# Kernel tuning notes

Measured on AMD Instinct MI355X. Metric: run time of the kernel, lower is better.

The kernel has to match this reference:

```python
import jax, jax.numpy as jnp
import numpy as np

N, E, F_IN, HID, H1, H2, H3, OUT = 10000, 160000, 50, 350, 4, 4, 6, 121


def _gat(x, src, dst, n, W, a_s, a_d, b, heads, C, concat):
    # PyG GATConv (dropout=0, eval): h = xW^T reshaped to [N,H,C]
    h = (x @ W.T).reshape(n, heads, C)
    alpha_src = jnp.einsum('nhc,hc->nh', h, a_s)  # [N,H]
    alpha_dst = jnp.einsum('nhc,hc->nh', h, a_d)  # [N,H]
    e = jax.nn.leaky_relu(alpha_src[src] + alpha_dst[dst], 0.2)  # [E,H]
    # numerically-stable segment softmax over incoming edges of each dst node
    m = jax.ops.segment_max(e, dst, num_segments=n)
    ee = jnp.exp(e - m[dst])
    s = jax.ops.segment_sum(ee, dst, num_segments=n)
    alpha = ee / s[dst]  # self-loops guarantee s > 0
    out = jax.ops.segment_sum(h[src] * alpha[:, :, None], dst, num_segments=n)  # [N,H,C]
    out = out.reshape(n, heads * C) if concat else out.mean(axis=1)
    return out + b


def setup_inputs() -> dict:
    key = jax.random.key(0)
    ks = jax.random.split(key, 16)
    sc = 0.05
    inp = {
        'x': jax.random.normal(ks[0], (N, F_IN), dtype=jnp.float32),
        'edge_index': jax.random.randint(ks[1], (2, E), 0, N, dtype=jnp.int64) if jax.config.jax_enable_x64 else jax.random.randint(ks[1], (2, E), 0, N, dtype=jnp.int32),
        'W1': jax.random.normal(ks[2], (H1 * HID, F_IN), dtype=jnp.float32) * sc,
        'a1s': jax.random.normal(ks[3], (H1, HID), dtype=jnp.float32) * sc,
        'a1d': jax.random.normal(ks[4], (H1, HID), dtype=jnp.float32) * sc,
        'b1': jnp.zeros((H1 * HID,), dtype=jnp.float32),
        'W2': jax.random.normal(ks[5], (H2 * HID, H1 * HID), dtype=jnp.float32) * sc,
        'a2s': jax.random.normal(ks[6], (H2, HID), dtype=jnp.float32) * sc,
        'a2d': jax.random.normal(ks[7], (H2, HID), dtype=jnp.float32) * sc,
        'b2': jnp.zeros((H2 * HID,), dtype=jnp.float32),
        'Wskip': jax.random.normal(ks[8], (H2 * HID, H1 * HID), dtype=jnp.float32) * sc,
        'W3': jax.random.normal(ks[9], (H3 * OUT, H2 * HID), dtype=jnp.float32) * sc,
        'a3s': jax.random.normal(ks[10], (H3, OUT), dtype=jnp.float32) * sc,
        'a3d': jax.random.normal(ks[11], (H3, OUT), dtype=jnp.float32) * sc,
        'b3': jnp.zeros((OUT,), dtype=jnp.float32),
    }
    return inp


def reference(x, edge_index, W1, a1s, a1d, b1, W2, a2s, a2d, b2, Wskip, W3, a3s, a3d, b3):
    n = x.shape[0]
    loops = jnp.arange(n, dtype=edge_index.dtype)  # PyG add_self_loops=True
    src = jnp.concatenate([edge_index[0], loops])
    dst = jnp.concatenate([edge_index[1], loops])
    h = jax.nn.elu(_gat(x, src, dst, n, W1, a1s, a1d, b1, H1, HID, True))
    x_in = h
    h = jax.nn.elu(_gat(h, src, dst, n, W2, a2s, a2d, b2, H2, HID, True))
    h = h + x_in @ Wskip.T  # skip connection (bias=False)
    return _gat(h, src, dst, n, W3, a3s, a3d, b3, H3, OUT, False)
```

## Files before the change

kernel.cpp:

```cpp
#include <hip/hip_runtime.h>
#include <math.h>

#define NNODES 10000
#define NEDGES 160000
#define E2 (NEDGES + NNODES)
#define F_IN 50
#define HIDC 350
#define NH1 4
#define NH2 4
#define NH3 6
#define OUTC 121
#define MAXE 96
#define KP1 64
#define KP2 1408
#define LD3 736
#define ROWSLACK 128

typedef __attribute__((ext_vector_type(8))) short short8;
typedef __attribute__((ext_vector_type(8))) unsigned short ushort8v;
typedef __attribute__((ext_vector_type(4))) float floatx4;

static __device__ __forceinline__ unsigned short f2bf(float f) {
    unsigned u = __float_as_uint(f);
    unsigned r = (u + 0x7fffu + ((u >> 16) & 1u)) >> 16;
    return (unsigned short)r;
}
static __device__ __forceinline__ float bf2f(unsigned short s) {
    return __uint_as_float(((unsigned)s) << 16);
}

#define GLL16(gp, lp)                                                      \
    __builtin_amdgcn_global_load_lds(                                      \
        (const __attribute__((address_space(1))) void*)(gp),               \
        (__attribute__((address_space(3))) void*)(lp), 16, 0, 0)

__global__ void count_kernel(const int* __restrict__ ei, int* __restrict__ cnt) {
    int i = blockIdx.x * blockDim.x + threadIdx.x;
    if (i >= E2) return;
    int dst = (i < NEDGES) ? ei[NEDGES + i] : (i - NEDGES);
    atomicAdd(&cnt[dst], 1);
}

__global__ void scan_kernel(const int* __restrict__ cnt, int* __restrict__ indptr,
                            int* __restrict__ cursor) {
    __shared__ int part[1024];
    int tid = threadIdx.x;
    const int CH = (NNODES + 1023) / 1024;
    int base = tid * CH;
    int s = 0;
    for (int i = 0; i < CH; i++) {
        int idx = base + i;
        if (idx < NNODES) s += cnt[idx];
    }
    part[tid] = s;
    __syncthreads();
    for (int off = 1; off < 1024; off <<= 1) {
        int v = (tid >= off) ? part[tid - off] : 0;
        __syncthreads();
        part[tid] += v;
        __syncthreads();
    }
    int run = (tid == 0) ? 0 : part[tid - 1];
    for (int i = 0; i < CH; i++) {
        int idx = base + i;
        if (idx < NNODES) {
            indptr[idx] = run;
            cursor[idx] = run;
            run += cnt[idx];
        }
    }
    if (tid == 0) indptr[NNODES] = part[1023];
}

__global__ void scatter_kernel(const int* __restrict__ ei, int* __restrict__ cursor,
                               int* __restrict__ esrc) {
    int i = blockIdx.x * blockDim.x + threadIdx.x;
    if (i >= E2) return;
    int src, dst;
    if (i < NEDGES) {
        src = ei[i];
        dst = ei[NEDGES + i];
    } else {
        src = dst = i - NEDGES;
    }
    int pos = atomicAdd(&cursor[dst], 1);
    esrc[pos] = src;
}

__global__ void splitW1_kernel(const float* __restrict__ W1,
                               unsigned short* __restrict__ w1Hi,
                               unsigned short* __restrict__ w1Lo) {
    int k = threadIdx.x;
    int r = blockIdx.x;
    float v = (k < F_IN) ? W1[(size_t)r * F_IN + k] : 0.f;
    unsigned short h = f2bf(v);
    w1Hi[(size_t)r * KP1 + k] = h;
    w1Lo[(size_t)r * KP1 + k] = f2bf(v - bf2f(h));
}

__global__ void splitB_kernel(const float* __restrict__ W2, const float* __restrict__ Wsk,
                              const float* __restrict__ W3,
                              unsigned short* __restrict__ w2Hi,
                              unsigned short* __restrict__ w3Hi) {
    int k = blockIdx.x * blockDim.x + threadIdx.x;
    if (k >= KP2) return;
    int r = blockIdx.y;
    const int K = 1400;
    const float* src;
    unsigned short* hi;
    int row;
    if (r < 1400) { src = W2; row = r; hi = w2Hi; }
    else if (r < 2800) { src = Wsk; row = r - 1400; hi = w2Hi + (size_t)1400 * KP2; }
    else { src = W3; row = r - 2800; hi = w3Hi; }
    float v = (k < K) ? src[(size_t)row * K + k] : 0.f;
    hi[(size_t)row * KP2 + k] = f2bf(v);
}

__global__ void atil_kernel(const float* __restrict__ W, const float* __restrict__ av_s,
                            const float* __restrict__ av_d, float* __restrict__ outS,
                            float* __restrict__ outD, int C, int K, int cchunk) {
    int k = blockIdx.x * 64 + (threadIdx.x & 63);
    if (k >= K) return;
    int h = blockIdx.y;
    int c0 = blockIdx.z * cchunk;
    int c1 = c0 + cchunk;
    if (c1 > C) c1 = C;
    float ss = 0.f, dd = 0.f;
    for (int c = c0; c < c1; c++) {
        float wv = W[((size_t)h * C + c) * K + k];
        ss = fmaf(wv, av_s[h * C + c], ss);
        dd = fmaf(wv, av_d[h * C + c], dd);
    }
    atomicAdd(&outS[(size_t)h * K + k], ss);
    atomicAdd(&outD[(size_t)h * K + k], dd);
}

__global__ void splitAT2_kernel(const float* __restrict__ atall,
                                unsigned short* __restrict__ atHi,
                                unsigned short* __restrict__ atLo) {
    int k = blockIdx.x * 64 + threadIdx.x;
    int r = blockIdx.y;
    float v = 0.f;
    if (k < 1400) {
        if (r < 4) v = atall[400 + r * 1400 + k];
        else if (r < 8) v = atall[6000 + (r - 4) * 1400 + k];
    }
    unsigned short h = f2bf(v);
    atHi[(size_t)r * KP2 + k] = h;
    atLo[(size_t)r * KP2 + k] = f2bf(v - bf2f(h));
}

__global__ __launch_bounds__(256) void alpha1x_kernel(const float* __restrict__ x,
                                                      const float* __restrict__ at1s,
                                                      const float* __restrict__ at1d,
                                                      float* __restrict__ as1,
                                                      float* __restrict__ ad1) {
    int wave = threadIdx.x >> 6, lane = threadIdx.x & 63;
    int n = blockIdx.x * 4 + wave;
    if (n >= NNODES) return;
    int kk = lane < F_IN ? lane : F_IN - 1;
    float v = (lane < F_IN) ? x[(size_t)n * F_IN + lane] : 0.f;
    float p[8];
#pragma unroll
    for (int h = 0; h < 4; h++) {
        p[h] = v * at1s[h * F_IN + kk];
        p[4 + h] = v * at1d[h * F_IN + kk];
    }
#pragma unroll
    for (int s = 0; s < 8; s++)
#pragma unroll
        for (int o = 32; o > 0; o >>= 1) p[s] += __shfl_xor(p[s], o, 64);
    if (lane == 0) {
#pragma unroll
        for (int h = 0; h < 4; h++) {
            as1[n * 4 + h] = p[h];
            ad1[n * 4 + h] = p[4 + h];
        }
    }
}

__global__ void zeropad_kernel(unsigned short* __restrict__ hi) {
    int i = blockIdx.x * 256 + threadIdx.x;
    if (i >= NNODES * 8) return;
    int n = i >> 3, c = 1400 + (i & 7);
    hi[(size_t)n * KP2 + c] = 0;
}

__global__ __launch_bounds__(256) void agg_x(
    const float* __restrict__ x, const float* __restrict__ as_n,
    const float* __restrict__ ad_n, const int* __restrict__ indptr,
    const int* __restrict__ esrc, unsigned short* __restrict__ xaggHi,
    unsigned short* __restrict__ xaggLo) {
    int n = blockIdx.x, tid = threadIdx.x;
    int s = indptr[n], e = indptr[n + 1];
    int deg = e - s;
    if (deg > MAXE) deg = MAXE;
    __shared__ int srcs[MAXE];
    __shared__ float wgt[MAXE * 4];

    if (tid < 64) {
        int lane = tid;
        float adv[4], mx[4], sm[4];
#pragma unroll
        for (int h = 0; h < 4; h++) {
            adv[h] = ad_n[n * 4 + h];
            mx[h] = -1e30f;
            sm[h] = 0.f;
        }
        for (int j = lane; j < deg; j += 64) {
            int sr = esrc[s + j];
            srcs[j] = sr;
#pragma unroll
            for (int h = 0; h < 4; h++) {
                float ev = as_n[sr * 4 + h] + adv[h];
                ev = ev > 0.f ? ev : 0.2f * ev;
                wgt[j * 4 + h] = ev;
                mx[h] = fmaxf(mx[h], ev);
            }
        }
#pragma unroll
        for (int h = 0; h < 4; h++)
#pragma unroll
            for (int o = 32; o > 0; o >>= 1) mx[h] = fmaxf(mx[h], __shfl_xor(mx[h], o, 64));
        for (int j = lane; j < deg; j += 64) {
#pragma unroll
            for (int h = 0; h < 4; h++) {
                float p = __expf(wgt[j * 4 + h] - mx[h]);
                wgt[j * 4 + h] = p;
                sm[h] += p;
            }
        }
#pragma unroll
        for (int h = 0; h < 4; h++) {
#pragma unroll
            for (int o = 32; o > 0; o >>= 1) sm[h] += __shfl_xor(sm[h], o, 64);
            sm[h] = 1.f / sm[h];
        }
        for (int j = lane; j < deg; j += 64) {
#pragma unroll
            for (int h = 0; h < 4; h++) wgt[j * 4 + h] *= sm[h];
        }
    }
    __syncthreads();

    int h = tid >> 6, k = tid & 63;
    float a = 0.f;
    if (k < F_IN) {
        float a2 = 0.f;
        int j = 0;
        for (; j + 1 < deg; j += 2) {
            a = fmaf(wgt[j * 4 + h], x[(size_t)srcs[j] * F_IN + k], a);
            a2 = fmaf(wgt[(j + 1) * 4 + h], x[(size_t)srcs[j + 1] * F_IN + k], a2);
        }
        if (j < deg) a = fmaf(wgt[j * 4 + h], x[(size_t)srcs[j] * F_IN + k], a);
        a += a2;
    }
    unsigned short hi = f2bf(a);
    xaggHi[(size_t)n * 256 + tid] = hi;
    xaggLo[(size_t)n * 256 + tid] = f2bf(a - bf2f(hi));
}

__global__ __launch_bounds__(256, 2) void gemm_h1(
    const unsigned short* __restrict__ xaggHi, const unsigned short* __restrict__ xaggLo,
    const unsigned short* __restrict__ w1Hi, const unsigned short* __restrict__ w1Lo,
    const float* __restrict__ bias, unsigned short* __restrict__ actHi) {
    __shared__ __align__(16) unsigned short sA[2][128 * 32];
    __shared__ __align__(16) unsigned short sB[2][256 * 32];
    int tid = threadIdx.x;
    int wave = tid >> 6, lane = tid & 63;
    int wm = (wave >> 1) * 64, wn = (wave & 1) * 128;
    int fr = lane & 15, kq = lane >> 4;
    int row0 = blockIdx.y * 128, col0 = blockIdx.x * 256;
    int hd = blockIdx.z;

    floatx4 acc[4][8];
#pragma unroll
    for (int i = 0; i < 4; i++)
#pragma unroll
        for (int j = 0; j < 8; j++)
#pragma unroll
            for (int q = 0; q < 4; q++) acc[i][j][q] = 0.f;

    int gpos = lane & 3;
    int rl = lane >> 2;
    int gsw = kq ^ ((fr >> 1) & 3);

    for (int k0 = 0; k0 < 64; k0 += 32) {
#pragma unroll
        for (int c = 0; c < 2; ++c) {
            int r = wave * 32 + c * 16 + rl;
            int g = gpos ^ ((r >> 1) & 3);
            size_t gofs = (size_t)(row0 + r) * 256 + hd * 64 + k0 + g * 8;
            size_t lofs = (size_t)r * 32 + (size_t)gpos * 8;
            GLL16(xaggHi + gofs, &sA[0][lofs]);
            GLL16(xaggLo + gofs, &sA[1][lofs]);
        }
#pragma unroll
        for (int c = 0; c < 4; ++c) {
            int r = wave * 64 + c * 16 + rl;
            int g = gpos ^ ((r >> 1) & 3);
            size_t gofs = (size_t)(hd * 350 + col0 + r) * KP1 + k0 + g * 8;
            size_t lofs = (size_t)r * 32 + (size_t)gpos * 8;
            GLL16(w1Hi + gofs, &sB[0][lofs]);
            GLL16(w1Lo + gofs, &sB[1][lofs]);
        }
        __syncthreads();

        short8 ah[4], al[4], bh[8], bl[8];
#pragma unroll
        for (int j = 0; j < 8; j++) {
            int rb = wn + j * 16 + fr;
            bh[j] = *(const short8*)&sB[0][rb * 32 + gsw * 8];
            bl[j] = *(const short8*)&sB[1][rb * 32 + gsw * 8];
        }
#pragma unroll
        for (int i = 0; i < 4; i++) {
            int ra = wm + i * 16 + fr;
            ah[i] = *(const short8*)&sA[0][ra * 32 + gsw * 8];
            al[i] = *(const short8*)&sA[1][ra * 32 + gsw * 8];
        }
#pragma unroll
        for (int i = 0; i < 4; i++)
#pragma unroll
            for (int j = 0; j < 8; j++) {
                acc[i][j] = __builtin_amdgcn_mfma_f32_16x16x32_bf16(ah[i], bh[j],
                                                                   acc[i][j], 0, 0, 0);
                acc[i][j] = __builtin_amdgcn_mfma_f32_16x16x32_bf16(al[i], bh[j],
                                                                   acc[i][j], 0, 0, 0);
                acc[i][j] = __builtin_amdgcn_mfma_f32_16x16x32_bf16(ah[i], bl[j],
                                                                   acc[i][j], 0, 0, 0);
            }
        __syncthreads();
    }

#pragma unroll
    for (int i = 0; i < 4; i++) {
#pragma unroll
        for (int rg = 0; rg < 4; rg++) {
            int rr = row0 + wm + i * 16 + kq * 4 + rg;
            if (rr >= NNODES) continue;
#pragma unroll
            for (int j = 0; j < 8; j++) {
                int cc = col0 + wn + j * 16 + fr;
                if (cc < 350) {
                    int gc = hd * 350 + cc;
                    float v = acc[i][j][rg] + bias[gc];
                    v = v > 0.f ? v : expm1f(v);
                    actHi[(size_t)rr * KP2 + gc] = f2bf(v);
                }
            }
        }
    }
}

__global__ __launch_bounds__(256) void alpha_mfma(
    const unsigned short* __restrict__ act, const unsigned short* __restrict__ tHi,
    const unsigned short* __restrict__ tLo, int H, float* __restrict__ asx,
    float* __restrict__ adx) {
    int wave = threadIdx.x >> 6, lane = threadIdx.x & 63;
    int row0 = (blockIdx.x * 4 + wave) * 16;
    if (row0 >= NNODES) return;
    int fr = lane & 15, kq = lane >> 4;
    floatx4 acc = {0.f, 0.f, 0.f, 0.f};
    const unsigned short* arow = act + (size_t)(row0 + fr) * KP2 + kq * 8;
    const unsigned short* brh = tHi + (size_t)fr * KP2 + kq * 8;
    const unsigned short* brl = tLo + (size_t)fr * KP2 + kq * 8;
#pragma unroll 4
    for (int k0 = 0; k0 < KP2; k0 += 32) {
        short8 a = *(const short8*)(arow + k0);
        short8 vh = *(const short8*)(brh + k0);
        short8 vl = *(const short8*)(brl + k0);
        acc = __builtin_amdgcn_mfma_f32_16x16x32_bf16(a, vh, acc, 0, 0, 0);
        acc = __builtin_amdgcn_mfma_f32_16x16x32_bf16(a, vl, acc, 0, 0, 0);
    }
#pragma unroll
    for (int rg = 0; rg < 4; rg++) {
        int rr = row0 + kq * 4 + rg;
        if (fr < H) asx[rr * H + fr] = acc[rg];
        else if (fr < 2 * H) adx[rr * H + (fr - H)] = acc[rg];
    }
}

__global__ __launch_bounds__(256, 2) void gemm_b16(
    const unsigned short* __restrict__ A, const unsigned short* __restrict__ B,
    unsigned short* __restrict__ Cb, int NN, int M, int Kp, int ldc) {
    __shared__ __align__(16) unsigned short sA[128 * 32];
    __shared__ __align__(16) unsigned short sB[256 * 32];
    int tid = threadIdx.x;
    int wave = tid >> 6, lane = tid & 63;
    int wm = (wave >> 1) * 64, wn = (wave & 1) * 128;
    int fr = lane & 15, kq = lane >> 4;
    int row0 = blockIdx.y * 128, col0 = blockIdx.x * 256;

    floatx4 acc[4][8];
#pragma unroll
    for (int i = 0; i < 4; i++)
#pragma unroll
        for (int j = 0; j < 8; j++)
#pragma unroll
            for (int q = 0; q < 4; q++) acc[i][j][q] = 0.f;

    int gpos = lane & 3;
    int rl = lane >> 2;
    int gsw = kq ^ ((fr >> 1) & 3);

    for (int k0 = 0; k0 < Kp; k0 += 32) {
#pragma unroll
        for (int c = 0; c < 2; ++c) {
            int r = wave * 32 + c * 16 + rl;
            int g = gpos ^ ((r >> 1) & 3);
            GLL16(A + (size_t)(row0 + r) * Kp + k0 + g * 8,
                  &sA[(size_t)r * 32 + (size_t)gpos * 8]);
        }
#pragma unroll
        for (int c = 0; c < 4; ++c) {
            int r = wave * 64 + c * 16 + rl;
            int g = gpos ^ ((r >> 1) & 3);
            GLL16(B + (size_t)(col0 + r) * Kp + k0 + g * 8,
                  &sB[(size_t)r * 32 + (size_t)gpos * 8]);
        }
        __syncthreads();

        short8 ah[4], bh[8];
#pragma unroll
        for (int j = 0; j < 8; j++) {
            int rb = wn + j * 16 + fr;
            bh[j] = *(const short8*)&sB[rb * 32 + gsw * 8];
        }
#pragma unroll
        for (int i = 0; i < 4; i++) {
            int ra = wm + i * 16 + fr;
            ah[i] = *(const short8*)&sA[ra * 32 + gsw * 8];
        }
#pragma unroll
        for (int i = 0; i < 4; i++)
#pragma unroll
            for (int j = 0; j < 8; j++)
                acc[i][j] = __builtin_amdgcn_mfma_f32_16x16x32_bf16(ah[i], bh[j],
                                                                   acc[i][j], 0, 0, 0);
        __syncthreads();
    }

#pragma unroll
    for (int i = 0; i < 4; i++) {
#pragma unroll
        for (int rg = 0; rg < 4; rg++) {
            int rr = row0 + wm + i * 16 + kq * 4 + rg;
            if (rr >= NN) continue;
#pragma unroll
            for (int j = 0; j < 8; j++) {
                int cc = col0 + wn + j * 16 + fr;
                if (cc < M) Cb[(size_t)rr * ldc + cc] = f2bf(acc[i][j][rg]);
            }
        }
    }
}

#define AGG_T 192
template <int H, int C, int MODE, int DOELU, int SKIP, int HN>
__global__ __launch_bounds__(AGG_T) void agg2(
    const unsigned short* __restrict__ hpreb, int ldh,
    const float* __restrict__ as_n, const float* __restrict__ ad_n,
    const int* __restrict__ indptr, const int* __restrict__ esrc,
    const float* __restrict__ bias, unsigned short* __restrict__ outHi, int Kp,
    float* __restrict__ outF, const float* __restrict__ atns,
    const float* __restrict__ atnd, float* __restrict__ asx,
    float* __restrict__ adx) {
    constexpr int HC = H * C;
    int n = blockIdx.x;
    int tid = threadIdx.x;
    int s = indptr[n], e = indptr[n + 1];
    int deg = e - s;
    if (deg > MAXE) deg = MAXE;

    __shared__ int srcs[MAXE];
    __shared__ float wgt[MAXE * H];
    __shared__ float aggsh[MODE ? HC : 1];
    __shared__ float sAl[16];
    if (tid < 16) sAl[tid] = 0.f;

    if (tid < 64) {
        int lane = tid;
        float adv[H], mx[H], sm[H];
#pragma unroll
        for (int h = 0; h < H; h++) {
            adv[h] = ad_n[n * H + h];
            mx[h] = -1e30f;
            sm[h] = 0.f;
        }
        for (int j = lane; j < deg; j += 64) {
            int sr = esrc[s + j];
            srcs[j] = sr;
#pragma unroll
            for (int h = 0; h < H; h++) {
                float ev = as_n[sr * H + h] + adv[h];
                ev = ev > 0.f ? ev : 0.2f * ev;
                wgt[j * H + h] = ev;
                mx[h] = fmaxf(mx[h], ev);
            }
        }
#pragma unroll
        for (int h = 0; h < H; h++)
#pragma unroll
            for (int o = 32; o > 0; o >>= 1) mx[h] = fmaxf(mx[h], __shfl_xor(mx[h], o, 64));
        for (int j = lane; j < deg; j += 64) {
#pragma unroll
            for (int h = 0; h < H; h++) {
                float p = __expf(wgt[j * H + h] - mx[h]);
                wgt[j * H + h] = p;
                sm[h] += p;
            }
        }
#pragma unroll
        for (int h = 0; h < H; h++) {
#pragma unroll
            for (int o = 32; o > 0; o >>= 1) sm[h] += __shfl_xor(sm[h], o, 64);
            sm[h] = 1.f / sm[h];
        }
        for (int j = lane; j < deg; j += 64) {
#pragma unroll
            for (int h = 0; h < H; h++) wgt[j * H + h] *= sm[h];
        }
    }
    __syncthreads();

    if (MODE == 0) {
        constexpr int NV8 = HC / 8;
        constexpr int NP = (HN > 0) ? 2 * HN : 1;
        float p[NP];
#pragma unroll
        for (int q = 0; q < NP; q++) p[q] = 0.f;

        for (int c8 = tid; c8 < NV8; c8 += AGG_T) {
            int cb = c8 * 8;
            int h0 = cb / C;
            int sp = (h0 + 1) * C - cb;
            if (sp > 8) sp = 8;
            int h1 = (h0 + 1 < H) ? h0 + 1 : h0;
            float av[8];
#pragma unroll
            for (int q = 0; q < 8; q++) av[q] = 0.f;
            int j = 0;
            for (; j + 3 < deg; j += 4) {
                const ushort8v v0 = *(const ushort8v*)(hpreb + (size_t)srcs[j] * ldh + cb);
                const ushort8v v1 = *(const ushort8v*)(hpreb + (size_t)srcs[j + 1] * ldh + cb);
                const ushort8v v2 = *(const ushort8v*)(hpreb + (size_t)srcs[j + 2] * ldh + cb);
                const ushort8v v3 = *(const ushort8v*)(hpreb + (size_t)srcs[j + 3] * ldh + cb);
                float wa0 = wgt[j * H + h0], wa1 = wgt[j * H + h1];
                float wb0 = wgt[(j + 1) * H + h0], wb1 = wgt[(j + 1) * H + h1];
                float wc0 = wgt[(j + 2) * H + h0], wc1 = wgt[(j + 2) * H + h1];
                float wd0 = wgt[(j + 3) * H + h0], wd1 = wgt[(j + 3) * H + h1];
#pragma unroll
                for (int q = 0; q < 8; q++) av[q] = fmaf(q < sp ? wa0 : wa1, bf2f(v0[q]), av[q]);
#pragma unroll
                for (int q = 0; q < 8; q++) av[q] = fmaf(q < sp ? wb0 : wb1, bf2f(v1[q]), av[q]);
#pragma unroll
                for (int q = 0; q < 8; q++) av[q] = fmaf(q < sp ? wc0 : wc1, bf2f(v2[q]), av[q]);
#pragma unroll
                for (int q = 0; q < 8; q++) av[q] = fmaf(q < sp ? wd0 : wd1, bf2f(v3[q]), av[q]);
            }
            for (; j < deg; j++) {
                const ushort8v v0 = *(const ushort8v*)(hpreb + (size_t)srcs[j] * ldh + cb);
                float wa0 = wgt[j * H + h0], wa1 = wgt[j * H + h1];
#pragma unroll
                for (int q = 0; q < 8; q++) av[q] = fmaf(q < sp ? wa0 : wa1, bf2f(v0[q]), av[q]);
            }
#pragma unroll
            for (int q = 0; q < 8; q++) av[q] += bias[cb + q];
            if (DOELU) {
#pragma unroll
                for (int q = 0; q < 8; q++) av[q] = av[q] > 0.f ? av[q] : expm1f(av[q]);
            }
            if (SKIP) {
                const ushort8v sk = *(const ushort8v*)(hpreb + (size_t)n * ldh + 1400 + cb);
#pragma unroll
                for (int q = 0; q < 8; q++) av[q] += bf2f(sk[q]);
            }
            if (HN > 0) {
#pragma unroll
                for (int h = 0; h < HN; h++) {
                    float ss = 0.f, dd = 0.f;
#pragma unroll
                    for (int q = 0; q < 8; q++) {
                        ss = fmaf(av[q], atns[(size_t)h * HC + cb + q], ss);
                        dd = fmaf(av[q], atnd[(size_t)h * HC + cb + q], dd);
                    }
                    p[h] += ss;
                    p[HN + h] += dd;
                }
            }
            ushort8v hi8;
#pragma unroll
            for (int q = 0; q < 8; q++) hi8[q] = f2bf(av[q]);
            *(ushort8v*)(outHi + (size_t)n * Kp + cb) = hi8;
        }
        for (int c = HC + tid; c < Kp; c += AGG_T) outHi[(size_t)n * Kp + c] = 0;
        if (HN > 0) {
#pragma unroll
            for (int q = 0; q < NP; q++)
#pragma unroll
                for (int o = 32; o > 0; o >>= 1) p[q] += __shfl_xor(p[q], o, 64);
            if ((tid & 63) == 0) {
#pragma unroll
                for (int q = 0; q < NP; q++) atomicAdd(&sAl[q], p[q]);
            }
            __syncthreads();
            if (tid < HN) asx[n * HN + tid] = sAl[tid];
            else if (tid < 2 * HN) adx[n * HN + (tid - HN)] = sAl[tid];
        }
    } else {
        constexpr int NV8 = (HC + 7) / 8;
        for (int c8 = tid; c8 < NV8; c8 += AGG_T) {
            int cb = c8 * 8;
            int h0 = cb / C;
            if (h0 >= H) h0 = H - 1;
            int sp = (h0 + 1) * C - cb;
            if (sp > 8) sp = 8;
            int h1 = (h0 + 1 < H) ? h0 + 1 : h0;
            float av[8];
#pragma unroll
            for (int q = 0; q < 8; q++) av[q] = 0.f;
            int j = 0;
            for (; j + 3 < deg; j += 4) {
                const ushort8v v0 = *(const ushort8v*)(hpreb + (size_t)srcs[j] * ldh + cb);
                const ushort8v v1 = *(const ushort8v*)(hpreb + (size_t)srcs[j + 1] * ldh + cb);
                const ushort8v v2 = *(const ushort8v*)(hpreb + (size_t)srcs[j + 2] * ldh + cb);
                const ushort8v v3 = *(const ushort8v*)(hpreb + (size_t)srcs[j + 3] * ldh + cb);
                float wa0 = wgt[j * H + h0], wa1 = wgt[j * H + h1];
                float wb0 = wgt[(j + 1) * H + h0], wb1 = wgt[(j + 1) * H + h1];
                float wc0 = wgt[(j + 2) * H + h0], wc1 = wgt[(j + 2) * H + h1];
                float wd0 = wgt[(j + 3) * H + h0], wd1 = wgt[(j + 3) * H + h1];
#pragma unroll
                for (int q = 0; q < 8; q++) av[q] = fmaf(q < sp ? wa0 : wa1, bf2f(v0[q]), av[q]);
#pragma unroll
                for (int q = 0; q < 8; q++) av[q] = fmaf(q < sp ? wb0 : wb1, bf2f(v1[q]), av[q]);
#pragma unroll
                for (int q = 0; q < 8; q++) av[q] = fmaf(q < sp ? wc0 : wc1, bf2f(v2[q]), av[q]);
#pragma unroll
                for (int q = 0; q < 8; q++) av[q] = fmaf(q < sp ? wd0 : wd1, bf2f(v3[q]), av[q]);
            }
            for (; j < deg; j++) {
                const ushort8v v0 = *(const ushort8v*)(hpreb + (size_t)srcs[j] * ldh + cb);
                float wa0 = wgt[j * H + h0], wa1 = wgt[j * H + h1];
#pragma unroll
                for (int q = 0; q < 8; q++) av[q] = fmaf(q < sp ? wa0 : wa1, bf2f(v0[q]), av[q]);
            }
#pragma unroll
            for (int q = 0; q < 8; q++)
                if (cb + q < HC) aggsh[cb + q] = av[q];
        }
        __syncthreads();
        for (int c = tid; c < C; c += AGG_T) {
            float sres = 0.f;
#pragma unroll
            for (int h = 0; h < H; h++) sres += aggsh[h * C + c];
            outF[(size_t)n * C + c] = sres * (1.f / (float)H) + bias[c];
        }
    }
}

extern "C" void kernel_launch(void* const* d_in, const int* in_sizes, int n_in,
                              void* d_out, int out_size, void* d_ws, size_t ws_size,
                              hipStream_t stream) {
    const float* x = (const float*)d_in[0];
    const int* ei = (const int*)d_in[1];
    const float* W1 = (const float*)d_in[2];
    const float* a1s = (const float*)d_in[3];
    const float* a1d = (const float*)d_in[4];
    const float* b1 = (const float*)d_in[5];
    const float* W2 = (const float*)d_in[6];
    const float* a2s = (const float*)d_in[7];
    const float* a2d = (const float*)d_in[8];
    const float* b2 = (const float*)d_in[9];
    const float* Wsk = (const float*)d_in[10];
    const float* W3 = (const float*)d_in[11];
    const float* a3s = (const float*)d_in[12];
    const float* a3d = (const float*)d_in[13];
    const float* b3 = (const float*)d_in[14];
    float* out = (float*)d_out;

    char* w = (char*)d_ws;
    size_t off = 0;
    auto alloc = [&](size_t bytes) -> char* {
        char* p = w + off;
        off += (bytes + 255) & ~(size_t)255;
        return p;
    };
    unsigned short* hpreb = (unsigned short*)alloc((size_t)(NNODES + ROWSLACK) * 2800 * 2);
    unsigned short* actHi = (unsigned short*)alloc((size_t)(NNODES + ROWSLACK) * KP2 * 2);
    unsigned short* xaggHi = (unsigned short*)alloc((size_t)(NNODES + ROWSLACK) * 256 * 2);
    unsigned short* xaggLo = (unsigned short*)alloc((size_t)(NNODES + ROWSLACK) * 256 * 2);
    unsigned short* w1Hi = (unsigned short*)alloc((size_t)(1400 + 512) * KP1 * 2);
    unsigned short* w1Lo = (unsigned short*)alloc((size_t)(1400 + 512) * KP1 * 2);
    unsigned short* w2Hi = (unsigned short*)alloc((size_t)(2800 + ROWSLACK) * KP2 * 2);
    unsigned short* w3Hi = (unsigned short*)alloc((size_t)(726 + ROWSLACK) * KP2 * 2);
    unsigned short* at2Hi = (unsigned short*)alloc((size_t)16 * KP2 * 2);
    unsigned short* at2Lo = (unsigned short*)alloc((size_t)16 * KP2 * 2);
    float* atall = (float*)alloc((size_t)28400 * 4);
    int* cnt = (int*)alloc((size_t)(NNODES + 16) * 4);
    float* at1s = atall;
    float* at1d = atall + 200;
    float* at2s = atall + 400;
    float* at2d = atall + 6000;
    float* at3s = atall + 11600;
    float* at3d = atall + 20000;
    float* asP = (float*)alloc((size_t)NNODES * 6 * 4);
    float* adP = (float*)alloc((size_t)NNODES * 6 * 4);
    float* asQ = (float*)alloc((size_t)NNODES * 6 * 4);
    float* adQ = (float*)alloc((size_t)NNODES * 6 * 4);
    int* indptr = (int*)alloc((size_t)(NNODES + 16) * 4);
    int* cursor = (int*)alloc((size_t)(NNODES + 16) * 4);
    int* esrc = (int*)alloc((size_t)E2 * 4);

    size_t zbytes = (size_t)((char*)cnt - (char*)atall) + (NNODES + 16) * 4;
    hipMemsetAsync(atall, 0, zbytes, stream);

    splitW1_kernel<<<1400, 64, 0, stream>>>(W1, w1Hi, w1Lo);
    splitB_kernel<<<dim3(6, 2800 + 726), 256, 0, stream>>>(W2, Wsk, W3, w2Hi, w3Hi);
    atil_kernel<<<dim3(1, 4, 5), 64, 0, stream>>>(W1, a1s, a1d, at1s, at1d, HIDC, F_IN, 70);
    atil_kernel<<<dim3(22, 4, 5), 64, 0, stream>>>(W2, a2s, a2d, at2s, at2d, HIDC, 1400, 70);
    atil_kernel<<<dim3(22, 6, 4), 64, 0, stream>>>(W3, a3s, a3d, at3s, at3d, OUTC, 1400, 31);
    splitAT2_kernel<<<dim3(22, 16), 64, 0, stream>>>(atall, at2Hi, at2Lo);
    alpha1x_kernel<<<(NNODES + 3) / 4, 256, 0, stream>>>(x, at1s, at1d, asP, adP);

    count_kernel<<<(E2 + 255) / 256, 256, 0, stream>>>(ei, cnt);
    scan_kernel<<<1, 1024, 0, stream>>>(cnt, indptr, cursor);
    scatter_kernel<<<(E2 + 255) / 256, 256, 0, stream>>>(ei, cursor, esrc);

    zeropad_kernel<<<(NNODES * 8 + 255) / 256, 256, 0, stream>>>(actHi);

    dim3 blk(256);
    int gy = (NNODES + 127) / 128;

    agg_x<<<NNODES, 256, 0, stream>>>(x, asP, adP, indptr, esrc, xaggHi, xaggLo);
    gemm_h1<<<dim3(2, gy, 4), blk, 0, stream>>>(xaggHi, xaggLo, w1Hi, w1Lo, b1, actHi);
    alpha_mfma<<<(NNODES / 16 + 3) / 4, 256, 0, stream>>>(actHi, at2Hi, at2Lo, 4, asQ, adQ);

    {
        int M = 2800;
        dim3 grid((M + 255) / 256, gy);
        gemm_b16<<<grid, blk, 0, stream>>>(actHi, w2Hi, hpreb, NNODES, M, KP2, 2800);
        agg2<NH2, HIDC, 0, 1, 1, 6><<<NNODES, AGG_T, 0, stream>>>(
            hpreb, 2800, asQ, adQ, indptr, esrc, b2, actHi, KP2, nullptr,
            at3s, at3d, asP, adP);
    }
    {
        int M = NH3 * OUTC;
        dim3 grid((M + 255) / 256, gy);
        gemm_b16<<<grid, blk, 0, stream>>>(actHi, w3Hi, hpreb, NNODES, M, KP2, LD3);
        agg2<NH3, OUTC, 1, 0, 0, 0><<<NNODES, AGG_T, 0, stream>>>(
            hpreb, LD3, asP, adP, indptr, esrc, b3, nullptr, 0, out,
            nullptr, nullptr, nullptr, nullptr);
    }
}
```

Measured before the change: 635.1 us.

## Precompute edge softmax weights in separate kernel and remap GEMM blocks across XCDs

The per-node edge softmax moves out of the aggregation kernels into a separate alpha_edge kernel that writes normalized weights to a global buffer. The aggregation kernels then just load those weights, so all threads start gathering at once instead of waiting for a single wave to finish the softmax. gemm_b16 also remaps block IDs so that consecutive tiles land on the same XCD, which is meant to improve L2 reuse. The cost is extra kernel launches and an extra global write and read of the per-edge weights.

```diff
diff --git a/kernel.cpp b/kernel.cpp
--- a/kernel.cpp
+++ b/kernel.cpp
@@ -381,6 +381,61 @@
     }
 }
 
+template <int H>
+__global__ __launch_bounds__(64) void alpha_edge(
+    const float* __restrict__ as_n, const float* __restrict__ ad_n,
+    const int* __restrict__ indptr, const int* __restrict__ esrc,
+    float* __restrict__ walpha) {
+    int n = blockIdx.x;
+    int lane = threadIdx.x;
+    int s = indptr[n], e = indptr[n + 1];
+    int deg = e - s;
+    if (deg > MAXE) deg = MAXE;
+    __shared__ float wgt[MAXE * H];
+    float adv[H], mx[H], sm[H];
+#pragma unroll
+    for (int h = 0; h < H; h++) {
+        adv[h] = ad_n[n * H + h];
+        mx[h] = -1e30f;
+        sm[h] = 0.f;
+    }
+    for (int j = lane; j < deg; j += 64) {
+        int sr = esrc[s + j];
+#pragma unroll
+        for (int h = 0; h < H; h++) {
+            float ev = as_n[sr * H + h] + adv[h];
+            ev = ev > 0.f ? ev : 0.2f * ev;
+            wgt[j * H + h] = ev;
+            mx[h] = fmaxf(mx[h], ev);
+        }
+    }
+#pragma unroll
+    for (int h = 0; h < H; h++)
+#pragma unroll
+        for (int o = 32; o > 0; o >>= 1) mx[h] = fmaxf(mx[h], __shfl_xor(mx[h], o, 64));
+    for (int j = lane; j < deg; j += 64) {
+#pragma unroll
+        for (int h = 0; h < H; h++) {
+            float p = __expf(wgt[j * H + h] - mx[h]);
+            wgt[j * H + h] = p;
+            sm[h] += p;
+        }
+    }
+#pragma unroll
+    for (int h = 0; h < H; h++) {
+#pragma unroll
+        for (int o = 32; o > 0; o >>= 1) sm[h] += __shfl_xor(sm[h], o, 64);
+        sm[h] = 1.f / sm[h];
+    }
+    for (int j = lane; j < deg; j += 64) {
+#pragma unroll
+        for (int h = 0; h < H; h++) wgt[j * H + h] *= sm[h];
+    }
+    __syncthreads();
+    for (int i = lane; i < deg * H; i += 64)
+        walpha[(size_t)s * H + i] = wgt[i];
+}
+
 __global__ __launch_bounds__(256, 2) void gemm_b16(
     const unsigned short* __restrict__ A, const unsigned short* __restrict__ B,
     unsigned short* __restrict__ Cb, int NN, int M, int Kp, int ldc) {
@@ -390,7 +445,14 @@
     int wave = tid >> 6, lane = tid & 63;
     int wm = (wave >> 1) * 64, wn = (wave & 1) * 128;
     int fr = lane & 15, kq = lane >> 4;
-    int row0 = blockIdx.y * 128, col0 = blockIdx.x * 256;
+
+    int gx = (int)gridDim.x;
+    int nwg = gx * (int)gridDim.y;
+    int bid = (int)blockIdx.y * gx + (int)blockIdx.x;
+    int qq = nwg >> 3, rr8 = nwg & 7;
+    int xcd = bid & 7, idx = bid >> 3;
+    int nb = (xcd < rr8) ? xcd * (qq + 1) + idx : rr8 * (qq + 1) + (xcd - rr8) * qq + idx;
+    int row0 = (nb / gx) * 128, col0 = (nb % gx) * 256;
 
     floatx4 acc[4][8];
 #pragma unroll
@@ -445,27 +507,122 @@
     for (int i = 0; i < 4; i++) {
 #pragma unroll
         for (int rg = 0; rg < 4; rg++) {
-            int rr = row0 + wm + i * 16 + kq * 4 + rg;
-            if (rr >= NN) continue;
+            int rrow = row0 + wm + i * 16 + kq * 4 + rg;
+            if (rrow >= NN) continue;
 #pragma unroll
             for (int j = 0; j < 8; j++) {
                 int cc = col0 + wn + j * 16 + fr;
-                if (cc < M) Cb[(size_t)rr * ldc + cc] = f2bf(acc[i][j][rg]);
+                if (cc < M) Cb[(size_t)rrow * ldc + cc] = f2bf(acc[i][j][rg]);
             }
         }
     }
 }
 
 #define AGG_T 192
-template <int H, int C, int MODE, int DOELU, int SKIP, int HN>
 __global__ __launch_bounds__(AGG_T) void agg2(
     const unsigned short* __restrict__ hpreb, int ldh,
-    const float* __restrict__ as_n, const float* __restrict__ ad_n,
     const int* __restrict__ indptr, const int* __restrict__ esrc,
-    const float* __restrict__ bias, unsigned short* __restrict__ outHi, int Kp,
-    float* __restrict__ outF, const float* __restrict__ atns,
-    const float* __restrict__ atnd, float* __restrict__ asx,
-    float* __restrict__ adx) {
+    const float* __restrict__ walpha, const float* __restrict__ bias,
+    unsigned short* __restrict__ outHi, int Kp,
+    const float* __restrict__ atns, const float* __restrict__ atnd,
+    float* __restrict__ asx, float* __restrict__ adx) {
+    constexpr int H = 4, C = 350, HC = 1400, HN = 6;
+    int n = blockIdx.x;
+    int tid = threadIdx.x;
+    int s = indptr[n], e = indptr[n + 1];
+    int deg = e - s;
+    if (deg > MAXE) deg = MAXE;
+
+    __shared__ int srcs[MAXE];
+    __shared__ float wgt[MAXE * H];
+    __shared__ float sAl[16];
+    if (tid < 16) sAl[tid] = 0.f;
+    for (int i = tid; i < deg; i += AGG_T) srcs[i] = esrc[s + i];
+    for (int i = tid; i < deg * H; i += AGG_T) wgt[i] = walpha[(size_t)s * H + i];
+    __syncthreads();
+
+    constexpr int NV8 = HC / 8;
+    float p[2 * HN];
+#pragma unroll
+    for (int q = 0; q < 2 * HN; q++) p[q] = 0.f;
+
+    for (int c8 = tid; c8 < NV8; c8 += AGG_T) {
+        int cb = c8 * 8;
+        int h0 = cb / C;
+        int sp = (h0 + 1) * C - cb;
+        if (sp > 8) sp = 8;
+        int h1 = (h0 + 1 < H) ? h0 + 1 : h0;
+        float av[8];
+#pragma unroll
+        for (int q = 0; q < 8; q++) av[q] = 0.f;
+        int j = 0;
+        for (; j + 3 < deg; j += 4) {
+            const ushort8v v0 = *(const ushort8v*)(hpreb + (size_t)srcs[j] * ldh + cb);
+            const ushort8v v1 = *(const ushort8v*)(hpreb + (size_t)srcs[j + 1] * ldh + cb);
+            const ushort8v v2 = *(const ushort8v*)(hpreb + (size_t)srcs[j + 2] * ldh + cb);
+            const ushort8v v3 = *(const ushort8v*)(hpreb + (size_t)srcs[j + 3] * ldh + cb);
+            float wa0 = wgt[j * H + h0], wa1 = wgt[j * H + h1];
+            float wb0 = wgt[(j + 1) * H + h0], wb1 = wgt[(j + 1) * H + h1];
+            float wc0 = wgt[(j + 2) * H + h0], wc1 = wgt[(j + 2) * H + h1];
+            float wd0 = wgt[(j + 3) * H + h0], wd1 = wgt[(j + 3) * H + h1];
+#pragma unroll
+            for (int q = 0; q < 8; q++) av[q] = fmaf(q < sp ? wa0 : wa1, bf2f(v0[q]), av[q]);
+#pragma unroll
+            for (int q = 0; q < 8; q++) av[q] = fmaf(q < sp ? wb0 : wb1, bf2f(v1[q]), av[q]);
+#pragma unroll
+            for (int q = 0; q < 8; q++) av[q] = fmaf(q < sp ? wc0 : wc1, bf2f(v2[q]), av[q]);
+#pragma unroll
+            for (int q = 0; q < 8; q++) av[q] = fmaf(q < sp ? wd0 : wd1, bf2f(v3[q]), av[q]);
+        }
+        for (; j < deg; j++) {
+            const ushort8v v0 = *(const ushort8v*)(hpreb + (size_t)srcs[j] * ldh + cb);
+            float wa0 = wgt[j * H + h0], wa1 = wgt[j * H + h1];
+#pragma unroll
+            for (int q = 0; q < 8; q++) av[q] = fmaf(q < sp ? wa0 : wa1, bf2f(v0[q]), av[q]);
+        }
+#pragma unroll
+        for (int q = 0; q < 8; q++) av[q] += bias[cb + q];
+#pragma unroll
+        for (int q = 0; q < 8; q++) av[q] = av[q] > 0.f ? av[q] : expm1f(av[q]);
+        const ushort8v sk = *(const ushort8v*)(hpreb + (size_t)n * ldh + 1400 + cb);
+#pragma unroll
+        for (int q = 0; q < 8; q++) av[q] += bf2f(sk[q]);
+#pragma unroll
+        for (int h = 0; h < HN; h++) {
+            float ss = 0.f, dd = 0.f;
+#pragma unroll
+            for (int q = 0; q < 8; q++) {
+                ss = fmaf(av[q], atns[(size_t)h * HC + cb + q], ss);
+                dd = fmaf(av[q], atnd[(size_t)h * HC + cb + q], dd);
+            }
+            p[h] += ss;
+            p[HN + h] += dd;
+        }
+        ushort8v hi8;
+#pragma unroll
+        for (int q = 0; q < 8; q++) hi8[q] = f2bf(av[q]);
+        *(ushort8v*)(outHi + (size_t)n * Kp + cb) = hi8;
+    }
+    for (int c = HC + tid; c < Kp; c += AGG_T) outHi[(size_t)n * Kp + c] = 0;
+#pragma unroll
+    for (int q = 0; q < 2 * HN; q++)
+#pragma unroll
+        for (int o = 32; o > 0; o >>= 1) p[q] += __shfl_xor(p[q], o, 64);
+    if ((tid & 63) == 0) {
+#pragma unroll
+        for (int q = 0; q < 2 * HN; q++) atomicAdd(&sAl[q], p[q]);
+    }
+    __syncthreads();
+    if (tid < HN) asx[n * HN + tid] = sAl[tid];
+    else if (tid < 2 * HN) adx[n * HN + (tid - HN)] = sAl[tid];
+}
+
+template <int H, int C>
+__global__ __launch_bounds__(AGG_T) void agg3(
+    const unsigned short* __restrict__ hpreb, int ldh,
+    const int* __restrict__ indptr, const int* __restrict__ esrc,
+    const float* __restrict__ walpha, const float* __restrict__ bias,
+    float* __restrict__ outF) {
     constexpr int HC = H * C;
     int n = blockIdx.x;
     int tid = threadIdx.x;
@@ -475,187 +632,57 @@
 
     __shared__ int srcs[MAXE];
     __shared__ float wgt[MAXE * H];
-    __shared__ float aggsh[MODE ? HC : 1];
-    __shared__ float sAl[16];
-    if (tid < 16) sAl[tid] = 0.f;
-
-    if (tid < 64) {
-        int lane = tid;
-        float adv[H], mx[H], sm[H];
-#pragma unroll
-        for (int h = 0; h < H; h++) {
-            adv[h] = ad_n[n * H + h];
-            mx[h] = -1e30f;
-            sm[h] = 0.f;
-        }
-        for (int j = lane; j < deg; j += 64) {
-            int sr = esrc[s + j];
-            srcs[j] = sr;
-#pragma unroll
-            for (int h = 0; h < H; h++) {
-                float ev = as_n[sr * H + h] + adv[h];
-                ev = ev > 0.f ? ev : 0.2f * ev;
-                wgt[j * H + h] = ev;
-                mx[h] = fmaxf(mx[h], ev);
-            }
-        }
-#pragma unroll
-        for (int h = 0; h < H; h++)
-#pragma unroll
-            for (int o = 32; o > 0; o >>= 1) mx[h] = fmaxf(mx[h], __shfl_xor(mx[h], o, 64));
-        for (int j = lane; j < deg; j += 64) {
-#pragma unroll
-            for (int h = 0; h < H; h++) {
-                float p = __expf(wgt[j * H + h] - mx[h]);
-                wgt[j * H + h] = p;
-                sm[h] += p;
-            }
-        }
-#pragma unroll
-        for (int h = 0; h < H; h++) {
-#pragma unroll
-            for (int o = 32; o > 0; o >>= 1) sm[h] += __shfl_xor(sm[h], o, 64);
-            sm[h] = 1.f / sm[h];
-        }
-        for (int j = lane; j < deg; j += 64) {
-#pragma unroll
-            for (int h = 0; h < H; h++) wgt[j * H + h] *= sm[h];
-        }
-    }
+    __shared__ float aggsh[HC];
+    for (int i = tid; i < deg; i += AGG_T) srcs[i] = esrc[s + i];
+    for (int i = tid; i < deg * H; i += AGG_T) wgt[i] = walpha[(size_t)s * H + i];
     __syncthreads();
 
-    if (MODE == 0) {
-        constexpr int NV8 = HC / 8;
-        constexpr int NP = (HN > 0) ? 2 * HN : 1;
-        float p[NP];
-#pragma unroll
-        for (int q = 0; q < NP; q++) p[q] = 0.f;
-
-        for (int c8 = tid; c8 < NV8; c8 += AGG_T) {
-            int cb = c8 * 8;
-            int h0 = cb / C;
-            int sp = (h0 + 1) * C - cb;
-            if (sp > 8) sp = 8;
-            int h1 = (h0 + 1 < H) ? h0 + 1 : h0;
-            float av[8];
-#pragma unroll
-            for (int q = 0; q < 8; q++) av[q] = 0.f;
-            int j = 0;
-            for (; j + 3 < deg; j += 4) {
-                const ushort8v v0 = *(const ushort8v*)(hpreb + (size_t)srcs[j] * ldh + cb);
-                const ushort8v v1 = *(const ushort8v*)(hpreb + (size_t)srcs[j + 1] * ldh + cb);
-                const ushort8v v2 = *(const ushort8v*)(hpreb + (size_t)srcs[j + 2] * ldh + cb);
-                const ushort8v v3 = *(const ushort8v*)(hpreb + (size_t)srcs[j + 3] * ldh + cb);
-                float wa0 = wgt[j * H + h0], wa1 = wgt[j * H + h1];
-                float wb0 = wgt[(j + 1) * H + h0], wb1 = wgt[(j + 1) * H + h1];
-                float wc0 = wgt[(j + 2) * H + h0], wc1 = wgt[(j + 2) * H + h1];
-                float wd0 = wgt[(j + 3) * H + h0], wd1 = wgt[(j + 3) * H + h1];
-#pragma unroll
-                for (int q = 0; q < 8; q++) av[q] = fmaf(q < sp ? wa0 : wa1, bf2f(v0[q]), av[q]);
-#pragma unroll
-                for (int q = 0; q < 8; q++) av[q] = fmaf(q < sp ? wb0 : wb1, bf2f(v1[q]), av[q]);
-#pragma unroll
-                for (int q = 0; q < 8; q++) av[q] = fmaf(q < sp ? wc0 : wc1, bf2f(v2[q]), av[q]);
-#pragma unroll
-                for (int q = 0; q < 8; q++) av[q] = fmaf(q < sp ? wd0 : wd1, bf2f(v3[q]), av[q]);
-            }
-            for (; j < deg; j++) {
-                const ushort8v v0 = *(const ushort8v*)(hpreb + (size_t)srcs[j] * ldh + cb);
-                float wa0 = wgt[j * H + h0], wa1 = wgt[j * H + h1];
-#pragma unroll
-                for (int q = 0; q < 8; q++) av[q] = fmaf(q < sp ? wa0 : wa1, bf2f(v0[q]), av[q]);
-            }
-#pragma unroll
-            for (int q = 0; q < 8; q++) av[q] += bias[cb + q];
-            if (DOELU) {
-#pragma unroll
-                for (int q = 0; q < 8; q++) av[q] = av[q] > 0.f ? av[q] : expm1f(av[q]);
-            }
-            if (SKIP) {
-                const ushort8v sk = *(const ushort8v*)(hpreb + (size_t)n * ldh + 1400 + cb);
-#pragma unroll
-                for (int q = 0; q < 8; q++) av[q] += bf2f(sk[q]);
-            }
-            if (HN > 0) {
-#pragma unroll
-                for (int h = 0; h < HN; h++) {
-                    float ss = 0.f, dd = 0.f;
-#pragma unroll
-                    for (int q = 0; q < 8; q++) {
-                        ss = fmaf(av[q], atns[(size_t)h * HC + cb + q], ss);
-                        dd = fmaf(av[q], atnd[(size_t)h * HC + cb + q], dd);
-                    }
-                    p[h] += ss;
-                    p[HN + h] += dd;
-                }
-            }
-            ushort8v hi8;
-#pragma unroll
-            for (int q = 0; q < 8; q++) hi8[q] = f2bf(av[q]);
-            *(ushort8v*)(outHi + (size_t)n * Kp + cb) = hi8;
-        }
-        for (int c = HC + tid; c < Kp; c += AGG_T) outHi[(size_t)n * Kp + c] = 0;
-        if (HN > 0) {
-#pragma unroll
-            for (int q = 0; q < NP; q++)
-#pragma unroll
-                for (int o = 32; o > 0; o >>= 1) p[q] += __shfl_xor(p[q], o, 64);
-            if ((tid & 63) == 0) {
-#pragma unroll
-                for (int q = 0; q < NP; q++) atomicAdd(&sAl[q], p[q]);
-            }
-            __syncthreads();
-            if (tid < HN) asx[n * HN + tid] = sAl[tid];
-            else if (tid < 2 * HN) adx[n * HN + (tid - HN)] = sAl[tid];
-        }
-    } else {
-        constexpr int NV8 = (HC + 7) / 8;
-        for (int c8 = tid; c8 < NV8; c8 += AGG_T) {
-            int cb = c8 * 8;
-            int h0 = cb / C;
-            if (h0 >= H) h0 = H - 1;
-            int sp = (h0 + 1) * C - cb;
-            if (sp > 8) sp = 8;
-            int h1 = (h0 + 1 < H) ? h0 + 1 : h0;
-            float av[8];
-#pragma unroll
-            for (int q = 0; q < 8; q++) av[q] = 0.f;
-            int j = 0;
-            for (; j + 3 < deg; j += 4) {
-                const ushort8v v0 = *(const ushort8v*)(hpreb + (size_t)srcs[j] * ldh + cb);
-                const ushort8v v1 = *(const ushort8v*)(hpreb + (size_t)srcs[j + 1] * ldh + cb);
-                const ushort8v v2 = *(const ushort8v*)(hpreb + (size_t)srcs[j + 2] * ldh + cb);
-                const ushort8v v3 = *(const ushort8v*)(hpreb + (size_t)srcs[j + 3] * ldh + cb);
-                float wa0 = wgt[j * H + h0], wa1 = wgt[j * H + h1];
-                float wb0 = wgt[(j + 1) * H + h0], wb1 = wgt[(j + 1) * H + h1];
-                float wc0 = wgt[(j + 2) * H + h0], wc1 = wgt[(j + 2) * H + h1];
-                float wd0 = wgt[(j + 3) * H + h0], wd1 = wgt[(j + 3) * H + h1];
-#pragma unroll
-                for (int q = 0; q < 8; q++) av[q] = fmaf(q < sp ? wa0 : wa1, bf2f(v0[q]), av[q]);
-#pragma unroll
-                for (int q = 0; q < 8; q++) av[q] = fmaf(q < sp ? wb0 : wb1, bf2f(v1[q]), av[q]);
-#pragma unroll
-                for (int q = 0; q < 8; q++) av[q] = fmaf(q < sp ? wc0 : wc1, bf2f(v2[q]), av[q]);
-#pragma unroll
-                for (int q = 0; q < 8; q++) av[q] = fmaf(q < sp ? wd0 : wd1, bf2f(v3[q]), av[q]);
-            }
-            for (; j < deg; j++) {
-                const ushort8v v0 = *(const ushort8v*)(hpreb + (size_t)srcs[j] * ldh + cb);
-                float wa0 = wgt[j * H + h0], wa1 = wgt[j * H + h1];
-#pragma unroll
-                for (int q = 0; q < 8; q++) av[q] = fmaf(q < sp ? wa0 : wa1, bf2f(v0[q]), av[q]);
-            }
-#pragma unroll
-            for (int q = 0; q < 8; q++)
-                if (cb + q < HC) aggsh[cb + q] = av[q];
-        }
-        __syncthreads();
-        for (int c = tid; c < C; c += AGG_T) {
-            float sres = 0.f;
-#pragma unroll
-            for (int h = 0; h < H; h++) sres += aggsh[h * C + c];
-            outF[(size_t)n * C + c] = sres * (1.f / (float)H) + bias[c];
-        }
+    constexpr int NV8 = (HC + 7) / 8;
+    for (int c8 = tid; c8 < NV8; c8 += AGG_T) {
+        int cb = c8 * 8;
+        int h0 = cb / C;
+        if (h0 >= H) h0 = H - 1;
+        int sp = (h0 + 1) * C - cb;
+        if (sp > 8) sp = 8;
+        int h1 = (h0 + 1 < H) ? h0 + 1 : h0;
+        float av[8];
+#pragma unroll
+        for (int q = 0; q < 8; q++) av[q] = 0.f;
+        int j = 0;
+        for (; j + 3 < deg; j += 4) {
+            const ushort8v v0 = *(const ushort8v*)(hpreb + (size_t)srcs[j] * ldh + cb);
+            const ushort8v v1 = *(const ushort8v*)(hpreb + (size_t)srcs[j + 1] * ldh + cb);
+            const ushort8v v2 = *(const ushort8v*)(hpreb + (size_t)srcs[j + 2] * ldh + cb);
+            const ushort8v v3 = *(const ushort8v*)(hpreb + (size_t)srcs[j + 3] * ldh + cb);
+            float wa0 = wgt[j * H + h0], wa1 = wgt[j * H + h1];
+            float wb0 = wgt[(j + 1) * H + h0], wb1 = wgt[(j + 1) * H + h1];
+            float wc0 = wgt[(j + 2) * H + h0], wc1 = wgt[(j + 2) * H + h1];
+            float wd0 = wgt[(j + 3) * H + h0], wd1 = wgt[(j + 3) * H + h1];
+#pragma unroll
+            for (int q = 0; q < 8; q++) av[q] = fmaf(q < sp ? wa0 : wa1, bf2f(v0[q]), av[q]);
+#pragma unroll
+            for (int q = 0; q < 8; q++) av[q] = fmaf(q < sp ? wb0 : wb1, bf2f(v1[q]), av[q]);
+#pragma unroll
+            for (int q = 0; q < 8; q++) av[q] = fmaf(q < sp ? wc0 : wc1, bf2f(v2[q]), av[q]);
+#pragma unroll
+            for (int q = 0; q < 8; q++) av[q] = fmaf(q < sp ? wd0 : wd1, bf2f(v3[q]), av[q]);
+        }
+        for (; j < deg; j++) {
+            const ushort8v v0 = *(const ushort8v*)(hpreb + (size_t)srcs[j] * ldh + cb);
+            float wa0 = wgt[j * H + h0], wa1 = wgt[j * H + h1];
+#pragma unroll
+            for (int q = 0; q < 8; q++) av[q] = fmaf(q < sp ? wa0 : wa1, bf2f(v0[q]), av[q]);
+        }
+#pragma unroll
+        for (int q = 0; q < 8; q++)
+            if (cb + q < HC) aggsh[cb + q] = av[q];
+    }
+    __syncthreads();
+    for (int c = tid; c < C; c += AGG_T) {
+        float sres = 0.f;
+#pragma unroll
+        for (int h = 0; h < H; h++) sres += aggsh[h * C + c];
+        outF[(size_t)n * C + c] = sres * (1.f / (float)H) + bias[c];
     }
 }
 
@@ -711,6 +738,7 @@
     int* indptr = (int*)alloc((size_t)(NNODES + 16) * 4);
     int* cursor = (int*)alloc((size_t)(NNODES + 16) * 4);
     int* esrc = (int*)alloc((size_t)E2 * 4);
+    float* walpha = (float*)alloc((size_t)E2 * 6 * 4);
 
     size_t zbytes = (size_t)((char*)cnt - (char*)atall) + (NNODES + 16) * 4;
     hipMemsetAsync(atall, 0, zbytes, stream);
@@ -735,21 +763,21 @@
     agg_x<<<NNODES, 256, 0, stream>>>(x, asP, adP, indptr, esrc, xaggHi, xaggLo);
     gemm_h1<<<dim3(2, gy, 4), blk, 0, stream>>>(xaggHi, xaggLo, w1Hi, w1Lo, b1, actHi);
     alpha_mfma<<<(NNODES / 16 + 3) / 4, 256, 0, stream>>>(actHi, at2Hi, at2Lo, 4, asQ, adQ);
+    alpha_edge<4><<<NNODES, 64, 0, stream>>>(asQ, adQ, indptr, esrc, walpha);
 
     {
         int M = 2800;
         dim3 grid((M + 255) / 256, gy);
         gemm_b16<<<grid, blk, 0, stream>>>(actHi, w2Hi, hpreb, NNODES, M, KP2, 2800);
-        agg2<NH2, HIDC, 0, 1, 1, 6><<<NNODES, AGG_T, 0, stream>>>(
-            hpreb, 2800, asQ, adQ, indptr, esrc, b2, actHi, KP2, nullptr,
-            at3s, at3d, asP, adP);
+        agg2<<<NNODES, AGG_T, 0, stream>>>(hpreb, 2800, indptr, esrc, walpha, b2,
+                                           actHi, KP2, at3s, at3d, asP, adP);
     }
     {
+        alpha_edge<6><<<NNODES, 64, 0, stream>>>(asP, adP, indptr, esrc, walpha);
         int M = NH3 * OUTC;
         dim3 grid((M + 255) / 256, gy);
         gemm_b16<<<grid, blk, 0, stream>>>(actHi, w3Hi, hpreb, NNODES, M, KP2, LD3);
-        agg2<NH3, OUTC, 1, 0, 0, 0><<<NNODES, AGG_T, 0, stream>>>(
-            hpreb, LD3, asP, adP, indptr, esrc, b3, nullptr, 0, out,
-            nullptr, nullptr, nullptr, nullptr);
-    }
-}
+        agg3<NH3, OUTC><<<NNODES, AGG_T, 0, stream>>>(
+            hpreb, LD3, indptr, esrc, walpha, b3, out);
+    }
+}
```

After: 628.0 us. About the same (-1.1%).
